# Kernel tuning notes

Hardware: AMD Instinct MI355X
Metric: run time of the kernel (lower is better)

Reference implementation:

```python
import jax, jax.numpy as jnp
import numpy as np

B, LQ, LKV, D = 32, 1024, 1024, 512

def setup_inputs() -> dict:
    key = jax.random.key(0)
    kq, kkv = jax.random.split(key)
    query = jax.random.normal(kq, (B, LQ, D), dtype=jnp.float32)
    key_value = jax.random.normal(kkv, (B, LKV, D), dtype=jnp.float32)
    return {"query": query, "key_value": key_value}

def reference(query, key_value):
    # scores: [B, Lq, Lkv] (unscaled dot-product attention)
    scores = jnp.einsum('bqd,bkd->bqk', query, key_value)
    attn_score = jax.nn.softmax(scores, axis=-1)
    # output: [B, Lq, D]
    output = jnp.einsum('bqk,bkd->bqd', attn_score, key_value)
    return (output, attn_score)
```

## Files before the change

### kernel.cpp

```cpp
#include <hip/hip_runtime.h>


constexpr int NB  = 32;
constexpr int LQ  = 1024;
constexpr int LKV = 1024;
constexpr int DD  = 512;
constexpr int NROWS = NB * LQ;

typedef __attribute__((ext_vector_type(4))) float f4;
typedef __attribute__((ext_vector_type(4))) float f32x4;
typedef __attribute__((ext_vector_type(4))) unsigned short u16x4;
typedef __attribute__((ext_vector_type(8))) __bf16 bf16x8;

__device__ __forceinline__ unsigned short f2bf(float x) {
  unsigned u = __builtin_bit_cast(unsigned, x);
  unsigned r = u + 0x7FFFu + ((u >> 16) & 1u);
  return (unsigned short)(r >> 16);
}
__device__ __forceinline__ float bf2f(unsigned short h) {
  unsigned u = ((unsigned)h) << 16;
  return __builtin_bit_cast(float, u);
}

__device__ __forceinline__ void gload16(const void* g, void* l) {
  __builtin_amdgcn_global_load_lds((const __attribute__((address_space(1))) unsigned int*)g,
                                   (__attribute__((address_space(3))) unsigned int*)l,
                                   16, 0, 0);
}

constexpr int PAD = 40;

__global__ __launch_bounds__(256) void prep_all_kernel(const float* __restrict__ Q,
                                                       const float* __restrict__ KV,
                                                       unsigned short* __restrict__ Qh,
                                                       unsigned short* __restrict__ Ql,
                                                       unsigned short* __restrict__ Kh,
                                                       unsigned short* __restrict__ Kl,
                                                       unsigned short* __restrict__ KVT)
{
  __shared__ unsigned short T[64][72];
  const int b  = blockIdx.z;
  const int tk = blockIdx.y;
  const int td = blockIdx.x;
  const int tid = threadIdx.x;

#pragma unroll
  for (int i = 0; i < 4; ++i) {
    int idx = tid + i * 256;
    int r   = idx >> 4;
    int c4  = (idx & 15) << 2;
    size_t goff = ((size_t)b * LKV + tk * 64 + r) * DD + td * 64 + c4;
    f4 v = *(const f4*)(KV + goff);
    u16x4 h, l;
#pragma unroll
    for (int u = 0; u < 4; ++u) {
      h[u] = f2bf(v[u]);
      l[u] = f2bf(v[u] - bf2f(h[u]));
    }
    *(u16x4*)&T[r][c4] = h;
    *(u16x4*)(Kh + goff) = h;
    *(u16x4*)(Kl + goff) = l;

    f4 q = *(const f4*)(Q + goff);
    u16x4 qh, ql;
#pragma unroll
    for (int u = 0; u < 4; ++u) {
      qh[u] = f2bf(q[u]);
      ql[u] = f2bf(q[u] - bf2f(qh[u]));
    }
    *(u16x4*)(Qh + goff) = qh;
    *(u16x4*)(Ql + goff) = ql;
  }
  __syncthreads();

#pragma unroll
  for (int i = 0; i < 4; ++i) {
    int idx = tid + i * 256;
    int c   = idx >> 4;
    int r4  = (idx & 15) << 2;
    u16x4 w = { T[r4][c], T[r4 + 1][c], T[r4 + 2][c], T[r4 + 3][c] };
    *(u16x4*)(KVT + ((size_t)b * DD + td * 64 + c) * LKV + tk * 64 + r4) = w;
  }
}

__global__ __launch_bounds__(256) void gemm_qk5_kernel(const unsigned short* __restrict__ Qh,
                                                       const unsigned short* __restrict__ Ql,
                                                       const unsigned short* __restrict__ Kh,
                                                       const unsigned short* __restrict__ Kl,
                                                       float* __restrict__ S,
                                                       float* __restrict__ Pmax,
                                                       float* __restrict__ Psum)
{
  __shared__ unsigned short SM[2][4][128 * 32];
  const int b   = blockIdx.y;
  const int ti  = blockIdx.x >> 3;
  const int tj  = blockIdx.x & 7;
  const int tid  = threadIdx.x;
  const int lane = tid & 63;
  const int wid  = tid >> 6;
  const int wr = (wid >> 1) * 64;
  const int wc = (wid & 1) * 64;

  const size_t qo = ((size_t)b * LQ  + ti * 128) * DD;
  const size_t ko = ((size_t)b * LKV + tj * 128) * DD;
  const unsigned short* tb =
      (wid == 0) ? Qh + qo : (wid == 1) ? Ql + qo : (wid == 2) ? Kh + ko : Kl + ko;

  const int lr  = lane >> 2;
  const int ssw = (lane & 3) ^ ((lr >> 1) & 3);

  f32x4 acc[4][4] = {};

#pragma unroll
  for (int c = 0; c < 8; ++c) {
    const unsigned short* g = tb + (size_t)(c * 16 + lr) * DD + 0 + ssw * 8;
    gload16(g, &SM[0][wid][c * 512]);
  }
  __syncthreads();

  const int l15 = lane & 15;
  const int cl  = lane >> 4;
  const int swz = (cl ^ ((l15 >> 1) & 3)) << 3;

  for (int it = 0; it < 16; ++it) {
    const int cur = it & 1;
    if (it < 15) {
      const int ks = (it + 1) * 32;
#pragma unroll
      for (int c = 0; c < 8; ++c) {
        const unsigned short* g = tb + (size_t)(c * 16 + lr) * DD + ks + ssw * 8;
        gload16(g, &SM[cur ^ 1][wid][c * 512]);
      }
    }
    bf16x8 ah[4], al[4], bh[4], bl[4];
#pragma unroll
    for (int m = 0; m < 4; ++m) {
      int rr = wr + m * 16 + l15;
      int off = rr * 32 + swz;
      ah[m] = *(const bf16x8*)&SM[cur][0][off];
      al[m] = *(const bf16x8*)&SM[cur][1][off];
    }
#pragma unroll
    for (int n = 0; n < 4; ++n) {
      int rr = wc + n * 16 + l15;
      int off = rr * 32 + swz;
      bh[n] = *(const bf16x8*)&SM[cur][2][off];
      bl[n] = *(const bf16x8*)&SM[cur][3][off];
    }
    __builtin_amdgcn_s_setprio(1);
#pragma unroll
    for (int m = 0; m < 4; ++m)
#pragma unroll
      for (int n = 0; n < 4; ++n)
        acc[m][n] = __builtin_amdgcn_mfma_f32_16x16x32_bf16(ah[m], bh[n], acc[m][n], 0, 0, 0);
#pragma unroll
    for (int m = 0; m < 4; ++m)
#pragma unroll
      for (int n = 0; n < 4; ++n)
        acc[m][n] = __builtin_amdgcn_mfma_f32_16x16x32_bf16(ah[m], bl[n], acc[m][n], 0, 0, 0);
#pragma unroll
    for (int m = 0; m < 4; ++m)
#pragma unroll
      for (int n = 0; n < 4; ++n)
        acc[m][n] = __builtin_amdgcn_mfma_f32_16x16x32_bf16(al[m], bh[n], acc[m][n], 0, 0, 0);
    __builtin_amdgcn_s_setprio(0);
    __syncthreads();
  }

  float* Sb = S + (size_t)b * LQ * LKV;
#pragma unroll
  for (int m = 0; m < 4; ++m) {
    int row0 = ti * 128 + wr + m * 16 + ((lane >> 4) << 2);
#pragma unroll
    for (int n = 0; n < 4; ++n) {
      int col = tj * 128 + wc + n * 16 + (lane & 15);
#pragma unroll
      for (int j = 0; j < 4; ++j)
        Sb[(size_t)(row0 + j) * LKV + col] = acc[m][n][j];
    }
  }

  const int g16  = lane >> 4;
  const int l16  = lane & 15;
  const int wcid = wc >> 6;
#pragma unroll
  for (int m = 0; m < 4; ++m) {
#pragma unroll
    for (int j = 0; j < 4; ++j) {
      float rm = fmaxf(fmaxf(acc[m][0][j], acc[m][1][j]), fmaxf(acc[m][2][j], acc[m][3][j]));
#pragma unroll
      for (int off = 8; off >= 1; off >>= 1)
        rm = fmaxf(rm, __shfl_xor(rm, off));
      float se = 0.f;
#pragma unroll
      for (int n = 0; n < 4; ++n)
        se += __expf(acc[m][n][j] - rm);
#pragma unroll
      for (int off = 8; off >= 1; off >>= 1)
        se += __shfl_xor(se, off);
      if (l16 == 0) {
        int row  = ti * 128 + wr + m * 16 + g16 * 4 + j;
        size_t p = ((size_t)b * LQ + row) * 16 + tj * 2 + wcid;
        Pmax[p] = rm;
        Psum[p] = se;
      }
    }
  }
}

__global__ __launch_bounds__(256) void reduce_stats_kernel(const float* __restrict__ Pmax,
                                                           const float* __restrict__ Psum,
                                                           float* __restrict__ M,
                                                           float* __restrict__ Inv)
{
  int row = blockIdx.x * 256 + threadIdx.x;
  const float* pm = Pmax + (size_t)row * 16;
  const float* ps = Psum + (size_t)row * 16;
  float mx = pm[0];
#pragma unroll
  for (int i = 1; i < 16; ++i) mx = fmaxf(mx, pm[i]);
  float s = 0.f;
#pragma unroll
  for (int i = 0; i < 16; ++i) s += ps[i] * __expf(pm[i] - mx);
  M[row]   = mx;
  Inv[row] = 1.0f / s;
}

__global__ __launch_bounds__(1024, 4) void gemm_av7_kernel(float* __restrict__ Sio,
                                                           const unsigned short* __restrict__ KVT,
                                                           const float* __restrict__ Mrow,
                                                           const float* __restrict__ Invr,
                                                           float* __restrict__ O)
{
  __shared__ unsigned short Asm[128][72];
  __shared__ unsigned short Bsm[512 * 64];
  __shared__ float Ms[128], Is[128];
  const int b  = blockIdx.y;
  const int mi = blockIdx.x;
  const int tid  = threadIdx.x;
  const int lane = tid & 63;
  const int wid  = tid >> 6;
  const int wr  = (wid >> 2) * 32;
  const int wcb = (wid & 3) * 128;

  float* Sb = Sio + ((size_t)b * LQ + mi * 128) * LKV;
  const unsigned short* Bb = KVT + (size_t)b * DD * LKV;

  if (tid < 128) {
    int gr = b * LQ + mi * 128 + tid;
    Ms[tid] = Mrow[gr];
    Is[tid] = Invr[gr];
  }

  const int lr8 = lane >> 3;
  const int ssw = (lane & 7) ^ lr8;

  f32x4 acc[2][8] = {};

  for (int ks = 0; ks < LKV; ks += 64) {
    __syncthreads();
#pragma unroll
    for (int i = 0; i < 2; ++i) {
      int idx = tid + i * 1024;
      int r   = idx >> 4;
      int k4  = (idx & 15) << 2;
      float* ap = Sb + (size_t)r * LKV + ks + k4;
      f4 v = *(const f4*)ap;
      float mr = Ms[r], ir = Is[r];
      f4 p; u16x4 h;
#pragma unroll
      for (int u = 0; u < 4; ++u) {
        p[u] = __expf(v[u] - mr) * ir;
        h[u] = f2bf(p[u]);
      }
      *(f4*)ap = p;
      *(u16x4*)&Asm[r][k4] = h;
    }
#pragma unroll
    for (int c = 0; c < 4; ++c) {
      int cc = wid * 4 + c;
      int dd = cc * 8 + lr8;
      const unsigned short* g = Bb + (size_t)dd * LKV + ks + ssw * 8;
      gload16(g, &Bsm[cc * 512]);
    }
    __syncthreads();

#pragma unroll
    for (int kk = 0; kk < 64; kk += 32) {
      const int kf = kk + ((lane >> 4) << 3);
      const int cl = kf >> 3;
      bf16x8 af[2];
#pragma unroll
      for (int m = 0; m < 2; ++m)
        af[m] = *(const bf16x8*)&Asm[wr + m * 16 + (lane & 15)][kf];
#pragma unroll
      for (int h = 0; h < 2; ++h) {
        bf16x8 bfv[4];
#pragma unroll
        for (int nn = 0; nn < 4; ++nn) {
          int dd = wcb + (h * 4 + nn) * 16 + (lane & 15);
          int sp = cl ^ (dd & 7);
          bfv[nn] = *(const bf16x8*)&Bsm[dd * 64 + sp * 8];
        }
#pragma unroll
        for (int m = 0; m < 2; ++m)
#pragma unroll
          for (int nn = 0; nn < 4; ++nn)
            acc[m][h * 4 + nn] =
                __builtin_amdgcn_mfma_f32_16x16x32_bf16(af[m], bfv[nn], acc[m][h * 4 + nn], 0, 0, 0);
      }
    }
  }

  float* Ob = O + ((size_t)b * LQ + mi * 128) * DD;
#pragma unroll
  for (int m = 0; m < 2; ++m) {
    int r0 = wr + m * 16 + ((lane >> 4) << 2);
#pragma unroll
    for (int n = 0; n < 8; ++n) {
      int col = wcb + n * 16 + (lane & 15);
#pragma unroll
      for (int j = 0; j < 4; ++j)
        Ob[(size_t)(r0 + j) * DD + col] = acc[m][n][j];
    }
  }
}

__global__ __launch_bounds__(256) void gemm_qk_kernel(const float* __restrict__ Q,
                                                      const float* __restrict__ KV,
                                                      float* __restrict__ S)
{
  __shared__ unsigned short Ah[128][PAD], Al[128][PAD], Bh[128][PAD], Bl[128][PAD];
  const int b   = blockIdx.y;
  const int ti  = blockIdx.x >> 3;
  const int tj  = blockIdx.x & 7;
  const int tid  = threadIdx.x;
  const int lane = tid & 63;
  const int wid  = tid >> 6;
  const int wr = (wid >> 1) * 64;
  const int wc = (wid & 1) * 64;

  const float* Qb = Q  + (size_t)b * LQ  * DD + (size_t)ti * 128 * DD;
  const float* Kb = KV + (size_t)b * LKV * DD + (size_t)tj * 128 * DD;

  f32x4 acc[4][4] = {};

  for (int ks = 0; ks < DD; ks += 32) {
    __syncthreads();
#pragma unroll
    for (int i = 0; i < 4; ++i) {
      int idx = tid + i * 256;
      int r   = idx >> 3;
      int k4  = (idx & 7) << 2;
      f4 qa = *(const f4*)(Qb + (size_t)r * DD + ks + k4);
      f4 ka = *(const f4*)(Kb + (size_t)r * DD + ks + k4);
      u16x4 qh, ql, kh, kl;
#pragma unroll
      for (int u = 0; u < 4; ++u) {
        unsigned short h = f2bf(qa[u]);
        qh[u] = h;  ql[u] = f2bf(qa[u] - bf2f(h));
        unsigned short h2 = f2bf(ka[u]);
        kh[u] = h2; kl[u] = f2bf(ka[u] - bf2f(h2));
      }
      *(u16x4*)&Ah[r][k4] = qh;  *(u16x4*)&Al[r][k4] = ql;
      *(u16x4*)&Bh[r][k4] = kh;  *(u16x4*)&Bl[r][k4] = kl;
    }
    __syncthreads();

    const int kf = (lane >> 4) << 3;
    bf16x8 ah[4], al[4], bh[4], bl[4];
#pragma unroll
    for (int m = 0; m < 4; ++m) {
      int row = wr + m * 16 + (lane & 15);
      ah[m] = *(const bf16x8*)&Ah[row][kf];
      al[m] = *(const bf16x8*)&Al[row][kf];
    }
#pragma unroll
    for (int n = 0; n < 4; ++n) {
      int row = wc + n * 16 + (lane & 15);
      bh[n] = *(const bf16x8*)&Bh[row][kf];
      bl[n] = *(const bf16x8*)&Bl[row][kf];
    }
#pragma unroll
    for (int m = 0; m < 4; ++m)
#pragma unroll
      for (int n = 0; n < 4; ++n) {
        acc[m][n] = __builtin_amdgcn_mfma_f32_16x16x32_bf16(ah[m], bh[n], acc[m][n], 0, 0, 0);
        acc[m][n] = __builtin_amdgcn_mfma_f32_16x16x32_bf16(ah[m], bl[n], acc[m][n], 0, 0, 0);
        acc[m][n] = __builtin_amdgcn_mfma_f32_16x16x32_bf16(al[m], bh[n], acc[m][n], 0, 0, 0);
      }
  }

  float* Sb = S + (size_t)b * LQ * LKV;
#pragma unroll
  for (int m = 0; m < 4; ++m) {
    int row0 = ti * 128 + wr + m * 16 + ((lane >> 4) << 2);
#pragma unroll
    for (int n = 0; n < 4; ++n) {
      int col = tj * 128 + wc + n * 16 + (lane & 15);
#pragma unroll
      for (int j = 0; j < 4; ++j)
        Sb[(size_t)(row0 + j) * LKV + col] = acc[m][n][j];
    }
  }
}

__global__ __launch_bounds__(256) void softmax_kernel(float* __restrict__ S)
{
  __shared__ float redmax[4], redsum[4];
  const int tid = threadIdx.x;
  float* p = S + (size_t)blockIdx.x * LKV;

  f4 v = *(const f4*)(p + tid * 4);
  float mx = fmaxf(fmaxf(v[0], v[1]), fmaxf(v[2], v[3]));
#pragma unroll
  for (int off = 32; off >= 1; off >>= 1)
    mx = fmaxf(mx, __shfl_xor(mx, off));
  if ((tid & 63) == 0) redmax[tid >> 6] = mx;
  __syncthreads();
  mx = fmaxf(fmaxf(redmax[0], redmax[1]), fmaxf(redmax[2], redmax[3]));

  f4 e;
#pragma unroll
  for (int u = 0; u < 4; ++u) e[u] = __expf(v[u] - mx);
  float sm = e[0] + e[1] + e[2] + e[3];
#pragma unroll
  for (int off = 32; off >= 1; off >>= 1)
    sm += __shfl_xor(sm, off);
  if ((tid & 63) == 0) redsum[tid >> 6] = sm;
  __syncthreads();
  sm = redsum[0] + redsum[1] + redsum[2] + redsum[3];

  float inv = 1.0f / sm;
  f4 o = { e[0] * inv, e[1] * inv, e[2] * inv, e[3] * inv };
  *(f4*)(p + tid * 4) = o;
}

__global__ __launch_bounds__(256) void kvt_prep_kernel(const float* __restrict__ KV,
                                                       unsigned short* __restrict__ KVT)
{
  __shared__ unsigned short T[64][72];
  const int b  = blockIdx.z;
  const int tk = blockIdx.y;
  const int td = blockIdx.x;
  const int tid = threadIdx.x;

#pragma unroll
  for (int i = 0; i < 4; ++i) {
    int idx = tid + i * 256;
    int r   = idx >> 4;
    int c4  = (idx & 15) << 2;
    f4 v = *(const f4*)(KV + ((size_t)b * LKV + tk * 64 + r) * DD + td * 64 + c4);
    u16x4 h;
#pragma unroll
    for (int u = 0; u < 4; ++u) h[u] = f2bf(v[u]);
    *(u16x4*)&T[r][c4] = h;
  }
  __syncthreads();

#pragma unroll
  for (int i = 0; i < 4; ++i) {
    int idx = tid + i * 256;
    int c   = idx >> 4;
    int r4  = (idx & 15) << 2;
    u16x4 w = { T[r4][c], T[r4 + 1][c], T[r4 + 2][c], T[r4 + 3][c] };
    *(u16x4*)(KVT + ((size_t)b * DD + td * 64 + c) * LKV + tk * 64 + r4) = w;
  }
}

__global__ __launch_bounds__(512) void gemm_av2_kernel(const float* __restrict__ A,
                                                       const unsigned short* __restrict__ KVT,
                                                       float* __restrict__ O)
{
  __shared__ unsigned short Asm[128][72];
  __shared__ unsigned short Bsm[256 * 64];
  const int b  = blockIdx.z;
  const int mi = blockIdx.y;
  const int nj = blockIdx.x;
  const int tid  = threadIdx.x;
  const int lane = tid & 63;
  const int wid  = tid >> 6;
  const int wr = (wid >> 2) * 64;
  const int wc = (wid & 3) * 64;

  const float* Ab = A + (size_t)b * LQ * LKV + (size_t)mi * 128 * LKV;
  const unsigned short* Bb = KVT + ((size_t)b * DD + nj * 256) * LKV;

  f32x4 acc[4][4] = {};

  for (int ks = 0; ks < LKV; ks += 64) {
    __syncthreads();
#pragma unroll
    for (int i = 0; i < 4; ++i) {
      int idx = tid + i * 512;
      int r   = idx >> 4;
      int k4  = (idx & 15) << 2;
      f4 v = *(const f4*)(Ab + (size_t)r * LKV + ks + k4);
      u16x4 h;
#pragma unroll
      for (int u = 0; u < 4; ++u) h[u] = f2bf(v[u]);
      *(u16x4*)&Asm[r][k4] = h;
    }
#pragma unroll
    for (int c = 0; c < 4; ++c) {
      int cc = wid * 4 + c;
      int dd = cc * 8 + (lane >> 3);
      int ss = (lane & 7) ^ (dd & 7);
      const unsigned short* g = Bb + (size_t)dd * LKV + ks + ss * 8;
      gload16(g, &Bsm[cc * 512]);
    }
    __syncthreads();

#pragma unroll
    for (int kk = 0; kk < 64; kk += 32) {
      const int kf = kk + ((lane >> 4) << 3);
      const int cl = kf >> 3;
      bf16x8 af[4], bfv[4];
#pragma unroll
      for (int m = 0; m < 4; ++m)
        af[m] = *(const bf16x8*)&Asm[wr + m * 16 + (lane & 15)][kf];
#pragma unroll
      for (int n = 0; n < 4; ++n) {
        int dd = wc + n * 16 + (lane & 15);
        int sp = cl ^ (dd & 7);
        bfv[n] = *(const bf16x8*)&Bsm[dd * 64 + sp * 8];
      }
#pragma unroll
      for (int m = 0; m < 4; ++m)
#pragma unroll
        for (int n = 0; n < 4; ++n)
          acc[m][n] = __builtin_amdgcn_mfma_f32_16x16x32_bf16(af[m], bfv[n], acc[m][n], 0, 0, 0);
    }
  }

  float* Ob = O + (size_t)b * LQ * DD;
#pragma unroll
  for (int m = 0; m < 4; ++m) {
    int row0 = mi * 128 + wr + m * 16 + ((lane >> 4) << 2);
#pragma unroll
    for (int n = 0; n < 4; ++n) {
      int col = nj * 256 + wc + n * 16 + (lane & 15);
#pragma unroll
      for (int j = 0; j < 4; ++j)
        Ob[(size_t)(row0 + j) * DD + col] = acc[m][n][j];
    }
  }
}

__global__ __launch_bounds__(256) void gemm_av_kernel(const float* __restrict__ A,
                                                      const float* __restrict__ KV,
                                                      float* __restrict__ O)
{
  __shared__ unsigned short Ab[128][PAD], Bt[128][PAD];
  const int b  = blockIdx.z;
  const int mi = blockIdx.y;
  const int nj = blockIdx.x;
  const int tid  = threadIdx.x;
  const int lane = tid & 63;
  const int wid  = tid >> 6;
  const int wr = (wid >> 1) * 64;
  const int wc = (wid & 1) * 64;

  const float* Arow = A  + (size_t)b * LQ * LKV + (size_t)mi * 128 * LKV;
  const float* Kb   = KV + (size_t)b * LKV * DD;

  f32x4 acc[4][4] = {};

  for (int ks = 0; ks < LKV; ks += 32) {
    __syncthreads();
#pragma unroll
    for (int i = 0; i < 4; ++i) {
      int idx = tid + i * 256;
      {
        int r  = idx >> 3;
        int k4 = (idx & 7) << 2;
        f4 av = *(const f4*)(Arow + (size_t)r * LKV + ks + k4);
        u16x4 h;
#pragma unroll
        for (int u = 0; u < 4; ++u) h[u] = f2bf(av[u]);
        *(u16x4*)&Ab[r][k4] = h;
      }
      {
        int kr = idx >> 5;
        int c4 = (idx & 31) << 2;
        f4 kv = *(const f4*)(Kb + (size_t)(ks + kr) * DD + nj * 128 + c4);
        unsigned short hv[4];
#pragma unroll
        for (int u = 0; u < 4; ++u) hv[u] = f2bf(kv[u]);
#pragma unroll
        for (int u = 0; u < 4; ++u) {
          int uu = (u + kr) & 3;
          Bt[c4 + uu][kr] = hv[uu];
        }
      }
    }
    __syncthreads();

    const int kf = (lane >> 4) << 3;
    bf16x8 af[4], bfv[4];
#pragma unroll
    for (int m = 0; m < 4; ++m)
      af[m] = *(const bf16x8*)&Ab[wr + m * 16 + (lane & 15)][kf];
#pragma unroll
    for (int n = 0; n < 4; ++n)
      bfv[n] = *(const bf16x8*)&Bt[wc + n * 16 + (lane & 15)][kf];
#pragma unroll
    for (int m = 0; m < 4; ++m)
#pragma unroll
      for (int n = 0; n < 4; ++n)
        acc[m][n] = __builtin_amdgcn_mfma_f32_16x16x32_bf16(af[m], bfv[n], acc[m][n], 0, 0, 0);
  }

  float* Ob = O + (size_t)b * LQ * DD;
#pragma unroll
  for (int m = 0; m < 4; ++m) {
    int row0 = mi * 128 + wr + m * 16 + ((lane >> 4) << 2);
#pragma unroll
    for (int n = 0; n < 4; ++n) {
      int col = nj * 128 + wc + n * 16 + (lane & 15);
#pragma unroll
      for (int j = 0; j < 4; ++j)
        Ob[(size_t)(row0 + j) * DD + col] = acc[m][n][j];
    }
  }
}

extern "C" void kernel_launch(void* const* d_in, const int* in_sizes, int n_in,
                              void* d_out, int out_size, void* d_ws, size_t ws_size,
                              hipStream_t stream) {
  const float* Q  = (const float*)d_in[0];
  const float* KV = (const float*)d_in[1];
  float* out  = (float*)d_out;
  float* attn = out + (size_t)NB * LQ * DD;

  const size_t NQ  = (size_t)NB * LQ * DD;
  const size_t big_bytes = 5 * NQ * sizeof(unsigned short);
  const size_t kvt_bytes = NQ * sizeof(unsigned short);

  if (ws_size >= big_bytes) {
    unsigned short* Qh  = (unsigned short*)d_ws;
    unsigned short* Qlo = Qh  + NQ;
    unsigned short* Kh  = Qlo + NQ;
    unsigned short* Kl  = Kh  + NQ;
    unsigned short* KVT = Kl  + NQ;
    float* Pmax = out;
    float* Psum = out + (size_t)NROWS * 16;
    float* Mrow = (float*)Kh;
    float* Invr = Mrow + NROWS;

    prep_all_kernel<<<dim3(DD / 64, LKV / 64, NB), 256, 0, stream>>>(Q, KV, Qh, Qlo, Kh, Kl, KVT);
    gemm_qk5_kernel<<<dim3(64, NB), 256, 0, stream>>>(Qh, Qlo, Kh, Kl, attn, Pmax, Psum);
    reduce_stats_kernel<<<NROWS / 256, 256, 0, stream>>>(Pmax, Psum, Mrow, Invr);
    gemm_av7_kernel<<<dim3(LQ / 128, NB), 1024, 0, stream>>>(attn, KVT, Mrow, Invr, out);
  } else if (ws_size >= kvt_bytes) {
    unsigned short* KVT = (unsigned short*)d_ws;
    gemm_qk_kernel<<<dim3(64, NB), 256, 0, stream>>>(Q, KV, attn);
    kvt_prep_kernel<<<dim3(DD / 64, LKV / 64, NB), 256, 0, stream>>>(KV, KVT);
    softmax_kernel<<<dim3(NB * LQ), 256, 0, stream>>>(attn);
    gemm_av2_kernel<<<dim3(DD / 256, LQ / 128, NB), 512, 0, stream>>>(attn, KVT, out);
  } else {
    gemm_qk_kernel<<<dim3(64, NB), 256, 0, stream>>>(Q, KV, attn);
    softmax_kernel<<<dim3(NB * LQ), 256, 0, stream>>>(attn);
    gemm_av_kernel<<<dim3(DD / 128, LQ / 128, NB), 256, 0, stream>>>(attn, KV, out);
  }
}
```

Before: 315.1 us.

## Remap grids to XCD-local batch order and single-buffer QK shared memory

```diff
diff --git a/kernel.cpp b/kernel.cpp
--- a/kernel.cpp
+++ b/kernel.cpp
@@ -83,7 +83,7 @@
   }
 }
 
-__global__ __launch_bounds__(256) void gemm_qk5_kernel(const unsigned short* __restrict__ Qh,
+__global__ __launch_bounds__(256) void gemm_qk7_kernel(const unsigned short* __restrict__ Qh,
                                                        const unsigned short* __restrict__ Ql,
                                                        const unsigned short* __restrict__ Kh,
                                                        const unsigned short* __restrict__ Kl,
@@ -91,10 +91,13 @@
                                                        float* __restrict__ Pmax,
                                                        float* __restrict__ Psum)
 {
-  __shared__ unsigned short SM[2][4][128 * 32];
-  const int b   = blockIdx.y;
-  const int ti  = blockIdx.x >> 3;
-  const int tj  = blockIdx.x & 7;
+  __shared__ unsigned short SM[4][128 * 32];
+  const int n       = blockIdx.x;
+  const int logical = (n & 7) * 256 + (n >> 3);
+  const int b   = logical >> 6;
+  const int t   = logical & 63;
+  const int ti  = t >> 3;
+  const int tj  = t & 7;
   const int tid  = threadIdx.x;
   const int lane = tid & 63;
   const int wid  = tid >> 6;
@@ -109,62 +112,49 @@
   const int lr  = lane >> 2;
   const int ssw = (lane & 3) ^ ((lr >> 1) & 3);
 
+  const int l15 = lane & 15;
+  const int swz = ((lane >> 4) ^ ((l15 >> 1) & 3)) << 3;
+
   f32x4 acc[4][4] = {};
 
-#pragma unroll
-  for (int c = 0; c < 8; ++c) {
-    const unsigned short* g = tb + (size_t)(c * 16 + lr) * DD + 0 + ssw * 8;
-    gload16(g, &SM[0][wid][c * 512]);
-  }
-  __syncthreads();
-
-  const int l15 = lane & 15;
-  const int cl  = lane >> 4;
-  const int swz = (cl ^ ((l15 >> 1) & 3)) << 3;
-
   for (int it = 0; it < 16; ++it) {
-    const int cur = it & 1;
-    if (it < 15) {
-      const int ks = (it + 1) * 32;
-#pragma unroll
-      for (int c = 0; c < 8; ++c) {
-        const unsigned short* g = tb + (size_t)(c * 16 + lr) * DD + ks + ssw * 8;
-        gload16(g, &SM[cur ^ 1][wid][c * 512]);
-      }
-    }
+    const int ks = it * 32;
+    __syncthreads();
+#pragma unroll
+    for (int c = 0; c < 8; ++c) {
+      const unsigned short* g = tb + (size_t)(c * 16 + lr) * DD + ks + ssw * 8;
+      gload16(g, &SM[wid][c * 512]);
+    }
+    __syncthreads();
+
     bf16x8 ah[4], al[4], bh[4], bl[4];
 #pragma unroll
     for (int m = 0; m < 4; ++m) {
-      int rr = wr + m * 16 + l15;
-      int off = rr * 32 + swz;
-      ah[m] = *(const bf16x8*)&SM[cur][0][off];
-      al[m] = *(const bf16x8*)&SM[cur][1][off];
-    }
-#pragma unroll
-    for (int n = 0; n < 4; ++n) {
-      int rr = wc + n * 16 + l15;
-      int off = rr * 32 + swz;
-      bh[n] = *(const bf16x8*)&SM[cur][2][off];
-      bl[n] = *(const bf16x8*)&SM[cur][3][off];
-    }
-    __builtin_amdgcn_s_setprio(1);
+      int off = (wr + m * 16 + l15) * 32 + swz;
+      ah[m] = *(const bf16x8*)&SM[0][off];
+      al[m] = *(const bf16x8*)&SM[1][off];
+    }
+#pragma unroll
+    for (int nn = 0; nn < 4; ++nn) {
+      int off = (wc + nn * 16 + l15) * 32 + swz;
+      bh[nn] = *(const bf16x8*)&SM[2][off];
+      bl[nn] = *(const bf16x8*)&SM[3][off];
+    }
 #pragma unroll
     for (int m = 0; m < 4; ++m)
 #pragma unroll
-      for (int n = 0; n < 4; ++n)
-        acc[m][n] = __builtin_amdgcn_mfma_f32_16x16x32_bf16(ah[m], bh[n], acc[m][n], 0, 0, 0);
+      for (int nn = 0; nn < 4; ++nn)
+        acc[m][nn] = __builtin_amdgcn_mfma_f32_16x16x32_bf16(ah[m], bh[nn], acc[m][nn], 0, 0, 0);
 #pragma unroll
     for (int m = 0; m < 4; ++m)
 #pragma unroll
-      for (int n = 0; n < 4; ++n)
-        acc[m][n] = __builtin_amdgcn_mfma_f32_16x16x32_bf16(ah[m], bl[n], acc[m][n], 0, 0, 0);
+      for (int nn = 0; nn < 4; ++nn)
+        acc[m][nn] = __builtin_amdgcn_mfma_f32_16x16x32_bf16(ah[m], bl[nn], acc[m][nn], 0, 0, 0);
 #pragma unroll
     for (int m = 0; m < 4; ++m)
 #pragma unroll
-      for (int n = 0; n < 4; ++n)
-        acc[m][n] = __builtin_amdgcn_mfma_f32_16x16x32_bf16(al[m], bh[n], acc[m][n], 0, 0, 0);
-    __builtin_amdgcn_s_setprio(0);
-    __syncthreads();
+      for (int nn = 0; nn < 4; ++nn)
+        acc[m][nn] = __builtin_amdgcn_mfma_f32_16x16x32_bf16(al[m], bh[nn], acc[m][nn], 0, 0, 0);
   }
 
   float* Sb = S + (size_t)b * LQ * LKV;
@@ -172,11 +162,11 @@
   for (int m = 0; m < 4; ++m) {
     int row0 = ti * 128 + wr + m * 16 + ((lane >> 4) << 2);
 #pragma unroll
-    for (int n = 0; n < 4; ++n) {
-      int col = tj * 128 + wc + n * 16 + (lane & 15);
+    for (int nn = 0; nn < 4; ++nn) {
+      int col = tj * 128 + wc + nn * 16 + (lane & 15);
 #pragma unroll
       for (int j = 0; j < 4; ++j)
-        Sb[(size_t)(row0 + j) * LKV + col] = acc[m][n][j];
+        Sb[(size_t)(row0 + j) * LKV + col] = acc[m][nn][j];
     }
   }
 
@@ -193,8 +183,8 @@
         rm = fmaxf(rm, __shfl_xor(rm, off));
       float se = 0.f;
 #pragma unroll
-      for (int n = 0; n < 4; ++n)
-        se += __expf(acc[m][n][j] - rm);
+      for (int nn = 0; nn < 4; ++nn)
+        se += __expf(acc[m][nn][j] - rm);
 #pragma unroll
       for (int off = 8; off >= 1; off >>= 1)
         se += __shfl_xor(se, off);
@@ -235,8 +225,10 @@
   __shared__ unsigned short Asm[128][72];
   __shared__ unsigned short Bsm[512 * 64];
   __shared__ float Ms[128], Is[128];
-  const int b  = blockIdx.y;
-  const int mi = blockIdx.x;
+  const int n       = blockIdx.x;
+  const int logical = (n & 7) * 32 + (n >> 3);
+  const int b  = logical >> 3;
+  const int mi = logical & 7;
   const int tid  = threadIdx.x;
   const int lane = tid & 63;
   const int wid  = tid >> 6;
@@ -317,11 +309,11 @@
   for (int m = 0; m < 2; ++m) {
     int r0 = wr + m * 16 + ((lane >> 4) << 2);
 #pragma unroll
-    for (int n = 0; n < 8; ++n) {
-      int col = wcb + n * 16 + (lane & 15);
+    for (int nn = 0; nn < 8; ++nn) {
+      int col = wcb + nn * 16 + (lane & 15);
 #pragma unroll
       for (int j = 0; j < 4; ++j)
-        Ob[(size_t)(r0 + j) * DD + col] = acc[m][n][j];
+        Ob[(size_t)(r0 + j) * DD + col] = acc[m][nn][j];
     }
   }
 }
@@ -649,9 +641,9 @@
     float* Invr = Mrow + NROWS;
 
     prep_all_kernel<<<dim3(DD / 64, LKV / 64, NB), 256, 0, stream>>>(Q, KV, Qh, Qlo, Kh, Kl, KVT);
-    gemm_qk5_kernel<<<dim3(64, NB), 256, 0, stream>>>(Qh, Qlo, Kh, Kl, attn, Pmax, Psum);
+    gemm_qk7_kernel<<<dim3(2048), 256, 0, stream>>>(Qh, Qlo, Kh, Kl, attn, Pmax, Psum);
     reduce_stats_kernel<<<NROWS / 256, 256, 0, stream>>>(Pmax, Psum, Mrow, Invr);
-    gemm_av7_kernel<<<dim3(LQ / 128, NB), 1024, 0, stream>>>(attn, KVT, Mrow, Invr, out);
+    gemm_av7_kernel<<<dim3(256), 1024, 0, stream>>>(attn, KVT, Mrow, Invr, out);
   } else if (ws_size >= kvt_bytes) {
     unsigned short* KVT = (unsigned short*)d_ws;
     gemm_qk_kernel<<<dim3(64, NB), 256, 0, stream>>>(Q, KV, attn);
```

New measurement: 314.9 us. No clear change (-0.1%).
